# Performance work log

Hardware: AMD Instinct MI355X
Metric: run time of the kernel (lower is better)

## Reference

```python
import jax, jax.numpy as jnp
import numpy as np

D = 768      # d_model
H = 12       # num_heads
L = 2        # num_blocks
N = 3        # number of sequence domains
B = 64       # batch
S = 512      # per-domain sequence length
MULT = 4     # ffn hidden_mult
A = 1        # action_num


def setup_inputs() -> dict:
    key = jax.random.key(0)
    ks = jax.random.split(key, 16)
    def w(k, shape):
        return jax.random.normal(k, shape, jnp.float32) * 0.02
    return {
        "context": jax.random.normal(ks[0], (B, D), jnp.float32),
        "sequences": jax.random.normal(ks[1], (N, B, S, D), jnp.float32),
        "seq_lens": jnp.maximum(jax.random.randint(ks[2], (N, B), 0, S + 1), 1).astype(jnp.int32),
        # per-block (stacked over L) ContextBlock params
        "blk_qn_w": jnp.ones((L, D)), "blk_qn_b": jnp.zeros((L, D)),
        "blk_sn_w": jnp.ones((L, D)), "blk_sn_b": jnp.zeros((L, D)),
        "blk_in_w": w(ks[3], (L, 3 * D, D)), "blk_in_b": jnp.zeros((L, 3 * D)),
        "blk_out_w": w(ks[4], (L, D, D)), "blk_out_b": jnp.zeros((L, D)),
        "blk_gate_w": w(ks[5], (L, D, 2 * D)), "blk_gate_b": jnp.zeros((L, D)),
        "blk_ffn_ln_w": jnp.ones((L, D)), "blk_ffn_ln_b": jnp.zeros((L, D)),
        "blk_ffn_w1": w(ks[6], (L, MULT * D, D)), "blk_ffn_b1": jnp.zeros((L, MULT * D)),
        "blk_ffn_w2": w(ks[7], (L, D, MULT * D)), "blk_ffn_b2": jnp.zeros((L, D)),
        # output norm + classifier
        "out_norm_w": jnp.ones((D,)), "out_norm_b": jnp.zeros((D,)),
        "cls_ln_w": jnp.ones((D,)), "cls_ln_b": jnp.zeros((D,)),
        "cls_w1": w(ks[8], (MULT * D, D)), "cls_b1": jnp.zeros((MULT * D,)),
        "cls_w2": w(ks[9], (A, MULT * D)), "cls_b2": jnp.zeros((A,)),
    }


def _ln(x, w, b):
    m = x.mean(-1, keepdims=True)
    v = ((x - m) ** 2).mean(-1, keepdims=True)
    return (x - m) * jax.lax.rsqrt(v + 1e-5) * w + b


def _forward(context, sequences, pad,
             blk_qn_w, blk_qn_b, blk_sn_w, blk_sn_b,
             blk_in_w, blk_in_b, blk_out_w, blk_out_b,
             blk_gate_w, blk_gate_b,
             blk_ffn_ln_w, blk_ffn_ln_b, blk_ffn_w1, blk_ffn_b1, blk_ffn_w2, blk_ffn_b2,
             out_norm_w, out_norm_b, cls_ln_w, cls_ln_b, cls_w1, cls_b1, cls_w2, cls_b2):
    dh = D // H
    scale = 1.0 / np.sqrt(dh)
    for l in range(L):
        # length-1 query over context; all N domains handled in one batched attention
        q = _ln(context, blk_qn_w[l], blk_qn_b[l])                       # [B, D]
        kv = _ln(sequences, blk_sn_w[l], blk_sn_b[l])                    # [N, B, S, D]
        Wq, Wk, Wv = jnp.split(blk_in_w[l], 3, axis=0)
        bq, bk, bv = jnp.split(blk_in_b[l], 3)
        qh = (q @ Wq.T + bq).reshape(B, H, dh)
        kh = (jnp.einsum('nbsd,ed->nbse', kv, Wk) + bk).reshape(N, B, S, H, dh)
        vh = (jnp.einsum('nbsd,ed->nbse', kv, Wv) + bv).reshape(N, B, S, H, dh)
        scores = jnp.einsum('bhe,nbshe->nbhs', qh, kh) * scale           # [N, B, H, S]
        scores = jnp.where(pad[:, :, None, :], jnp.float32(-1e30), scores)
        attn = jax.nn.softmax(scores, axis=-1)
        ctx = jnp.einsum('nbhs,nbshe->nbhe', attn, vh).reshape(N, B, D)
        attended = ctx @ blk_out_w[l].T + blk_out_b[l]                   # [N, B, D]
        seq_ctx = attended.mean(axis=0)                                  # mean over domains
        gate = jax.nn.sigmoid(jnp.concatenate([context, seq_ctx], axis=-1) @ blk_gate_w[l].T + blk_gate_b[l])
        context = context + gate * seq_ctx
        h = _ln(context, blk_ffn_ln_w[l], blk_ffn_ln_b[l])
        h = jax.nn.silu(h @ blk_ffn_w1[l].T + blk_ffn_b1[l]) @ blk_ffn_w2[l].T + blk_ffn_b2[l]
        context = context + h
    emb = _ln(context, out_norm_w, out_norm_b)
    h = _ln(emb, cls_ln_w, cls_ln_b)
    return jax.nn.silu(h @ cls_w1.T + cls_b1) @ cls_w2.T + cls_b2        # [B, A]


def reference(context, sequences, seq_lens,
              blk_qn_w, blk_qn_b, blk_sn_w, blk_sn_b,
              blk_in_w, blk_in_b, blk_out_w, blk_out_b,
              blk_gate_w, blk_gate_b,
              blk_ffn_ln_w, blk_ffn_ln_b, blk_ffn_w1, blk_ffn_b1, blk_ffn_w2, blk_ffn_b2,
              out_norm_w, out_norm_b, cls_ln_w, cls_ln_b, cls_w1, cls_b1, cls_w2, cls_b2):
    pad = jnp.arange(S)[None, None, :] >= seq_lens[:, :, None]           # [N, B, S], True = padded
    return _forward(context, sequences, pad,
                    blk_qn_w, blk_qn_b, blk_sn_w, blk_sn_b,
                    blk_in_w, blk_in_b, blk_out_w, blk_out_b,
                    blk_gate_w, blk_gate_b,
                    blk_ffn_ln_w, blk_ffn_ln_b, blk_ffn_w1, blk_ffn_b1, blk_ffn_w2, blk_ffn_b2,
                    out_norm_w, out_norm_b, cls_ln_w, cls_ln_b, cls_w1, cls_b1, cls_w2, cls_b2)
```

## Files before the change

### kernel.cpp

```cpp
#include <hip/hip_runtime.h>
#include <hip/hip_bf16.h>
#include <cstdint>

#define DMODEL 768
#define NB 64
#define NHEAD 12
#define DHEAD 64
#define SEQLEN 512
#define NDOM 3
#define NBLK 2
#define FFNH 3072
#define NBROWS (NDOM*NB)
#define NCH 16
#define ROWCH 32

__device__ __forceinline__ float wsum64(float v){
  #pragma unroll
  for (int o = 32; o; o >>= 1) v += __shfl_xor(v, o, 64);
  return v;
}
__device__ __forceinline__ float wmax64(float v){
  #pragma unroll
  for (int o = 32; o; o >>= 1) v = fmaxf(v, __shfl_xor(v, o, 64));
  return v;
}
__device__ __forceinline__ float dot4f(float4 a, float4 b){
  return fmaf(a.x, b.x, fmaf(a.y, b.y, fmaf(a.z, b.z, a.w * b.w)));
}

__global__ __launch_bounds__(256) void k_ln(const float* __restrict__ in,
    const float* __restrict__ w, const float* __restrict__ b,
    float* __restrict__ out, int rows){
  int gw = (blockIdx.x * 256 + threadIdx.x) >> 6;
  int lane = threadIdx.x & 63;
  if (gw >= rows) return;
  const float4* x4 = (const float4*)(in + (size_t)gw * DMODEL);
  float4 v0 = x4[lane], v1 = x4[64 + lane], v2 = x4[128 + lane];
  float s = v0.x+v0.y+v0.z+v0.w + v1.x+v1.y+v1.z+v1.w + v2.x+v2.y+v2.z+v2.w;
  float q = dot4f(v0,v0) + dot4f(v1,v1) + dot4f(v2,v2);
  s = wsum64(s); q = wsum64(q);
  float m = s * (1.0f / DMODEL);
  float var = q * (1.0f / DMODEL) - m * m;
  float r = rsqrtf(var + 1e-5f);
  const float4* w4 = (const float4*)w;
  const float4* b4 = (const float4*)b;
  float4* o4 = (float4*)(out + (size_t)gw * DMODEL);
  float4 vv[3] = {v0, v1, v2};
  #pragma unroll
  for (int seg = 0; seg < 3; ++seg){
    float4 ww = w4[seg*64 + lane], bb = b4[seg*64 + lane], x = vv[seg], o;
    o.x = (x.x - m) * r * ww.x + bb.x;
    o.y = (x.y - m) * r * ww.y + bb.y;
    o.z = (x.z - m) * r * ww.z + bb.z;
    o.w = (x.w - m) * r * ww.w + bb.w;
    o4[seg*64 + lane] = o;
  }
}

__global__ __launch_bounds__(256) void k_ln2(const float* __restrict__ in,
    const float* __restrict__ w1, const float* __restrict__ b1,
    const float* __restrict__ w2, const float* __restrict__ b2,
    float* __restrict__ out, int rows){
  int gw = (blockIdx.x * 256 + threadIdx.x) >> 6;
  int lane = threadIdx.x & 63;
  if (gw >= rows) return;
  const float4* x4 = (const float4*)(in + (size_t)gw * DMODEL);
  float4 vv[3] = {x4[lane], x4[64 + lane], x4[128 + lane]};
  float s = 0, q = 0;
  #pragma unroll
  for (int g = 0; g < 3; ++g){
    s += vv[g].x+vv[g].y+vv[g].z+vv[g].w;
    q += dot4f(vv[g], vv[g]);
  }
  s = wsum64(s); q = wsum64(q);
  float m = s * (1.0f/DMODEL);
  float r = rsqrtf(q * (1.0f/DMODEL) - m*m + 1e-5f);
  const float4* w14 = (const float4*)w1; const float4* b14 = (const float4*)b1;
  float4 yy[3];
  float s2 = 0, q2 = 0;
  #pragma unroll
  for (int g = 0; g < 3; ++g){
    float4 ww = w14[g*64 + lane], bb = b14[g*64 + lane], x = vv[g], o;
    o.x = (x.x - m)*r*ww.x + bb.x; o.y = (x.y - m)*r*ww.y + bb.y;
    o.z = (x.z - m)*r*ww.z + bb.z; o.w = (x.w - m)*r*ww.w + bb.w;
    yy[g] = o;
    s2 += o.x+o.y+o.z+o.w; q2 += dot4f(o,o);
  }
  s2 = wsum64(s2); q2 = wsum64(q2);
  float m2 = s2 * (1.0f/DMODEL);
  float r2 = rsqrtf(q2 * (1.0f/DMODEL) - m2*m2 + 1e-5f);
  const float4* w24 = (const float4*)w2; const float4* b24 = (const float4*)b2;
  float4* o4 = (float4*)(out + (size_t)gw * DMODEL);
  #pragma unroll
  for (int g = 0; g < 3; ++g){
    float4 ww = w24[g*64 + lane], bb = b24[g*64 + lane], y = yy[g], o;
    o.x = (y.x - m2)*r2*ww.x + bb.x; o.y = (y.y - m2)*r2*ww.y + bb.y;
    o.z = (y.z - m2)*r2*ww.z + bb.z; o.w = (y.w - m2)*r2*ww.w + bb.w;
    o4[g*64 + lane] = o;
  }
}

template<int K, int NC, int ACT, bool RES>
__global__ __launch_bounds__(256) void k_gemmW(const float* __restrict__ A,
    const float* __restrict__ W, const float* __restrict__ bias,
    const float* __restrict__ res, float* __restrict__ out){
  int gw = (blockIdx.x * 256 + threadIdx.x) >> 6;
  int lane = threadIdx.x & 63;
  int sl = lane & 7, g = lane >> 3;
  int bg = gw & 7; int j0 = (gw >> 3) * 4;
  const float4* a4 = (const float4*)(A + (size_t)(bg*8 + g) * K);
  const float4* w0 = (const float4*)(W + (size_t)(j0+0) * K);
  const float4* w1 = (const float4*)(W + (size_t)(j0+1) * K);
  const float4* w2 = (const float4*)(W + (size_t)(j0+2) * K);
  const float4* w3 = (const float4*)(W + (size_t)(j0+3) * K);
  float acc0 = 0, acc1 = 0, acc2 = 0, acc3 = 0;
  #pragma unroll 4
  for (int i = 0; i < K/32; ++i){
    float4 av = a4[i*8 + sl];
    acc0 += dot4f(av, w0[i*8 + sl]);
    acc1 += dot4f(av, w1[i*8 + sl]);
    acc2 += dot4f(av, w2[i*8 + sl]);
    acc3 += dot4f(av, w3[i*8 + sl]);
  }
  #pragma unroll
  for (int o = 1; o <= 4; o <<= 1){
    acc0 += __shfl_xor(acc0, o, 64);
    acc1 += __shfl_xor(acc1, o, 64);
    acc2 += __shfl_xor(acc2, o, 64);
    acc3 += __shfl_xor(acc3, o, 64);
  }
  if (sl == 0){
    int row = bg*8 + g;
    float4 bj = *(const float4*)(bias + j0);
    float a[4] = {acc0, acc1, acc2, acc3};
    float bb[4] = {bj.x, bj.y, bj.z, bj.w};
    float v[4];
    #pragma unroll
    for (int u = 0; u < 4; ++u){
      float t = (ACT == 2) ? a[u] * (1.0f/3.0f) + bb[u] : a[u] + bb[u];
      if (ACT == 1) t = t / (1.0f + __expf(-t));
      v[u] = t;
    }
    size_t o = (size_t)row * NC + j0;
    if (RES){
      float4 rr = *(const float4*)(res + o);
      v[0] += rr.x; v[1] += rr.y; v[2] += rr.z; v[3] += rr.w;
    }
    *(float4*)(out + o) = make_float4(v[0], v[1], v[2], v[3]);
  }
}

__global__ __launch_bounds__(256) void k_qpr(const float* __restrict__ qh,
    const float* __restrict__ Wk, const float* __restrict__ snw,
    const float* __restrict__ snb, const float* __restrict__ bk,
    float* __restrict__ QW, float* __restrict__ SQW, float* __restrict__ SC){
  int w = (blockIdx.x * 256 + threadIdx.x) >> 6;
  int lane = threadIdx.x & 63;
  int b = w / NHEAD, h = w - b * NHEAD;
  const float* qrow = qh + (size_t)b * DMODEL + h * DHEAD;
  const float* wbase = Wk + (size_t)h * DHEAD * DMODEL;
  float qp[12] = {};
  for (int e = 0; e < DHEAD; ++e){
    float qv = qrow[e];
    const float* wr = wbase + (size_t)e * DMODEL;
    #pragma unroll
    for (int k = 0; k < 12; ++k) qp[k] = fmaf(qv, wr[k*64 + lane], qp[k]);
  }
  float s1 = 0, s2 = 0;
  float* qwout = QW + (size_t)w * DMODEL;
  #pragma unroll
  for (int k = 0; k < 12; ++k){
    int d = k*64 + lane;
    float q = qp[k];
    float qwv = q * snw[d] * 0.125f;
    qwout[d] = qwv;
    s1 += qwv;
    s2 = fmaf(q, snb[d], s2);
  }
  float s3 = qrow[lane] * bk[h*DHEAD + lane];
  s1 = wsum64(s1); s2 = wsum64(s2); s3 = wsum64(s3);
  if (lane == 0){ SQW[w] = s1; SC[w] = 0.125f * (s2 + s3); }
}

__global__ __launch_bounds__(256, 2) void k_attn4(const float* __restrict__ seq,
    const int* __restrict__ lens, const float* __restrict__ QW,
    const float* __restrict__ SQW, const float* __restrict__ SC,
    float* __restrict__ Pacc, float* __restrict__ Pden,
    float* __restrict__ Pc, float* __restrict__ Pmx){
  int blk = blockIdx.x;
  int ch = blk & (NCH-1); int nb = blk >> 4;
  int wid = threadIdx.x >> 6; int lane = threadIdx.x & 63;
  int b = nb % NB;
  int len = lens[nb];
  int s0 = ch * ROWCH;
  if (s0 >= len) return;
  int send = s0 + ROWCH < len ? s0 + ROWCH : len;
  int h0 = wid * 3;
  size_t pb = (size_t)blk * NHEAD + h0;
  const float4* qwb = (const float4*)(QW + ((size_t)b * NHEAD + h0) * DMODEL);
  float4 q0[3], q1[3], q2[3];
  #pragma unroll
  for (int j = 0; j < 3; ++j){
    q0[j] = qwb[j*(DMODEL/4) + lane];
    q1[j] = qwb[j*(DMODEL/4) + 64 + lane];
    q2[j] = qwb[j*(DMODEL/4) + 128 + lane];
  }
  float sqv[3], scv[3];
  #pragma unroll
  for (int j = 0; j < 3; ++j){ sqv[j] = SQW[b*NHEAD + h0 + j]; scv[j] = SC[b*NHEAD + h0 + j]; }
  float4 a0[3], a1[3], a2[3];
  #pragma unroll
  for (int j = 0; j < 3; ++j){
    a0[j] = make_float4(0,0,0,0); a1[j] = make_float4(0,0,0,0); a2[j] = make_float4(0,0,0,0);
  }
  float den[3] = {0,0,0}, cac[3] = {0,0,0}, mx[3] = {-3.0e38f,-3.0e38f,-3.0e38f};
  const float4* xr = (const float4*)(seq + ((size_t)nb * SEQLEN + s0) * DMODEL);
  float4 x0 = xr[lane], x1 = xr[64 + lane], x2 = xr[128 + lane];
  for (int s = s0; s < send; ++s){
    float4 c0 = x0, c1 = x1, c2 = x2;
    if (s + 1 < send){
      const float4* nx = (const float4*)(seq + ((size_t)nb * SEQLEN + s + 1) * DMODEL);
      x0 = nx[lane]; x1 = nx[64 + lane]; x2 = nx[128 + lane];
    }
    float sm = c0.x+c0.y+c0.z+c0.w + c1.x+c1.y+c1.z+c1.w + c2.x+c2.y+c2.z+c2.w;
    float qq = dot4f(c0,c0) + dot4f(c1,c1) + dot4f(c2,c2);
    float d0 = dot4f(q0[0],c0) + dot4f(q1[0],c1) + dot4f(q2[0],c2);
    float d1 = dot4f(q0[1],c0) + dot4f(q1[1],c1) + dot4f(q2[1],c2);
    float d2 = dot4f(q0[2],c0) + dot4f(q1[2],c1) + dot4f(q2[2],c2);
    sm = wsum64(sm); qq = wsum64(qq);
    d0 = wsum64(d0); d1 = wsum64(d1); d2 = wsum64(d2);
    float m = sm * (1.0f/DMODEL);
    float var = qq * (1.0f/DMODEL) - m * m;
    float r = rsqrtf(var + 1e-5f);
    float dt[3] = {d0, d1, d2};
    #pragma unroll
    for (int j = 0; j < 3; ++j){
      float score = r * (dt[j] - m * sqv[j]) + scv[j];
      if (score > mx[j] + 8.0f){
        float f = __expf(mx[j] - score);
        den[j] *= f; cac[j] *= f;
        a0[j].x*=f; a0[j].y*=f; a0[j].z*=f; a0[j].w*=f;
        a1[j].x*=f; a1[j].y*=f; a1[j].z*=f; a1[j].w*=f;
        a2[j].x*=f; a2[j].y*=f; a2[j].z*=f; a2[j].w*=f;
        mx[j] = score;
      }
      float e = __expf(score - mx[j]);
      float er = e * r;
      a0[j].x = fmaf(er, c0.x, a0[j].x); a0[j].y = fmaf(er, c0.y, a0[j].y);
      a0[j].z = fmaf(er, c0.z, a0[j].z); a0[j].w = fmaf(er, c0.w, a0[j].w);
      a1[j].x = fmaf(er, c1.x, a1[j].x); a1[j].y = fmaf(er, c1.y, a1[j].y);
      a1[j].z = fmaf(er, c1.z, a1[j].z); a1[j].w = fmaf(er, c1.w, a1[j].w);
      a2[j].x = fmaf(er, c2.x, a2[j].x); a2[j].y = fmaf(er, c2.y, a2[j].y);
      a2[j].z = fmaf(er, c2.z, a2[j].z); a2[j].w = fmaf(er, c2.w, a2[j].w);
      den[j] += e;
      cac[j] = fmaf(er, m, cac[j]);
    }
  }
  #pragma unroll
  for (int j = 0; j < 3; ++j){
    float4* pa = (float4*)(Pacc + (pb + j) * DMODEL);
    pa[lane] = a0[j]; pa[64 + lane] = a1[j]; pa[128 + lane] = a2[j];
    if (lane == 0){ Pden[pb+j] = den[j]; Pc[pb+j] = cac[j]; Pmx[pb+j] = mx[j]; }
  }
}

__global__ __launch_bounds__(256) void k_comb(const float* __restrict__ Pacc,
    const float* __restrict__ Pden, const float* __restrict__ Pc,
    const float* __restrict__ Pmx, const int* __restrict__ lens,
    const float* __restrict__ snw, const float* __restrict__ snb,
    float* __restrict__ wsum){
  int tid = blockIdx.x * 256 + threadIdx.x;
  int d = tid % DMODEL;
  int t = tid / DMODEL;
  int h = t % NHEAD;
  int b = t / NHEAD;
  float vec = 0.0f, csum = 0.0f;
  #pragma unroll
  for (int n = 0; n < NDOM; ++n){
    int nb = n*NB + b;
    int len = lens[nb];
    int na = (len + ROWCH - 1) >> 5; if (na > NCH) na = NCH;
    size_t p0 = (size_t)nb * NCH * NHEAD + h;
    float M = -3.0e38f;
    for (int c = 0; c < na; ++c) M = fmaxf(M, Pmx[p0 + (size_t)c*NHEAD]);
    float D = 0, V = 0, C = 0;
    for (int c = 0; c < na; ++c){
      size_t pi = p0 + (size_t)c*NHEAD;
      float w = __expf(Pmx[pi] - M);
      D = fmaf(w, Pden[pi], D);
      V = fmaf(w, Pacc[pi*DMODEL + d], V);
      C = fmaf(w, Pc[pi], C);
    }
    float inv = 1.0f / D;
    vec = fmaf(V, inv, vec);
    csum = fmaf(C, inv, csum);
  }
  wsum[tid] = (vec - csum) * snw[d] + 3.0f * snb[d];
}

__global__ __launch_bounds__(256) void k_ctxv2(const float* __restrict__ wsum,
    const float* __restrict__ Wv, const float* __restrict__ bv, float* __restrict__ ctxsum){
  int gw = (blockIdx.x * 256 + threadIdx.x) >> 6;
  int lane = threadIdx.x & 63;
  int sl = lane & 7, g = lane >> 3;
  int bg = gw & 7; int j0 = (gw >> 3) * 4;
  int h = j0 >> 6;
  const float4* a4 = (const float4*)(wsum + ((size_t)(bg*8 + g) * NHEAD + h) * DMODEL);
  const float4* w0 = (const float4*)(Wv + (size_t)(j0+0) * DMODEL);
  const float4* w1 = (const float4*)(Wv + (size_t)(j0+1) * DMODEL);
  const float4* w2 = (const float4*)(Wv + (size_t)(j0+2) * DMODEL);
  const float4* w3 = (const float4*)(Wv + (size_t)(j0+3) * DMODEL);
  float acc0 = 0, acc1 = 0, acc2 = 0, acc3 = 0;
  #pragma unroll 4
  for (int i = 0; i < DMODEL/32; ++i){
    float4 av = a4[i*8 + sl];
    acc0 += dot4f(av, w0[i*8 + sl]);
    acc1 += dot4f(av, w1[i*8 + sl]);
    acc2 += dot4f(av, w2[i*8 + sl]);
    acc3 += dot4f(av, w3[i*8 + sl]);
  }
  #pragma unroll
  for (int o = 1; o <= 4; o <<= 1){
    acc0 += __shfl_xor(acc0, o, 64);
    acc1 += __shfl_xor(acc1, o, 64);
    acc2 += __shfl_xor(acc2, o, 64);
    acc3 += __shfl_xor(acc3, o, 64);
  }
  if (sl == 0){
    float4 bb = *(const float4*)(bv + j0);
    float4 v = make_float4(acc0 + 3.0f*bb.x, acc1 + 3.0f*bb.y, acc2 + 3.0f*bb.z, acc3 + 3.0f*bb.w);
    *(float4*)(ctxsum + (size_t)(bg*8 + g) * DMODEL + j0) = v;
  }
}

__global__ __launch_bounds__(256) void k_gate2(const float* __restrict__ ctx,
    const float* __restrict__ sctx, const float* __restrict__ Wg,
    const float* __restrict__ gb, float* __restrict__ out){
  int gw = (blockIdx.x * 256 + threadIdx.x) >> 6;
  int lane = threadIdx.x & 63;
  int sl = lane & 7, g = lane >> 3;
  int bg = gw & 7; int j0 = (gw >> 3) * 4;
  int row = bg*8 + g;
  const float4* c4 = (const float4*)(ctx + (size_t)row * DMODEL);
  const float4* s4 = (const float4*)(sctx + (size_t)row * DMODEL);
  const float4* wr0 = (const float4*)(Wg + (size_t)(j0+0) * 2 * DMODEL);
  const float4* wr1 = (const float4*)(Wg + (size_t)(j0+1) * 2 * DMODEL);
  const float4* wr2 = (const float4*)(Wg + (size_t)(j0+2) * 2 * DMODEL);
  const float4* wr3 = (const float4*)(Wg + (size_t)(j0+3) * 2 * DMODEL);
  float acc0 = 0, acc1 = 0, acc2 = 0, acc3 = 0;
  #pragma unroll 4
  for (int i = 0; i < DMODEL/32; ++i){
    float4 cv = c4[i*8 + sl], sv = s4[i*8 + sl];
    acc0 += dot4f(cv, wr0[i*8 + sl]) + dot4f(sv, wr0[192 + i*8 + sl]);
    acc1 += dot4f(cv, wr1[i*8 + sl]) + dot4f(sv, wr1[192 + i*8 + sl]);
    acc2 += dot4f(cv, wr2[i*8 + sl]) + dot4f(sv, wr2[192 + i*8 + sl]);
    acc3 += dot4f(cv, wr3[i*8 + sl]) + dot4f(sv, wr3[192 + i*8 + sl]);
  }
  #pragma unroll
  for (int o = 1; o <= 4; o <<= 1){
    acc0 += __shfl_xor(acc0, o, 64);
    acc1 += __shfl_xor(acc1, o, 64);
    acc2 += __shfl_xor(acc2, o, 64);
    acc3 += __shfl_xor(acc3, o, 64);
  }
  if (sl == 0){
    size_t o = (size_t)row * DMODEL + j0;
    float4 bb = *(const float4*)(gb + j0);
    float4 cc = *(const float4*)(ctx + o);
    float4 ss = *(const float4*)(sctx + o);
    float4 v;
    v.x = cc.x + ss.x / (1.0f + __expf(-(acc0 + bb.x)));
    v.y = cc.y + ss.y / (1.0f + __expf(-(acc1 + bb.y)));
    v.z = cc.z + ss.z / (1.0f + __expf(-(acc2 + bb.z)));
    v.w = cc.w + ss.w / (1.0f + __expf(-(acc3 + bb.w)));
    *(float4*)(out + o) = v;
  }
}

__global__ __launch_bounds__(256) void k_cls2(const float* __restrict__ h2,
    const float* __restrict__ w2, const float* __restrict__ b2, float* __restrict__ out){
  int b = blockIdx.x; int t = threadIdx.x;
  float acc = 0;
  for (int j = t; j < FFNH; j += 256) acc = fmaf(h2[(size_t)b*FFNH + j], w2[j], acc);
  acc = wsum64(acc);
  __shared__ float sh[4];
  if ((t & 63) == 0) sh[t >> 6] = acc;
  __syncthreads();
  if (t == 0) out[b] = sh[0] + sh[1] + sh[2] + sh[3] + b2[0];
}

extern "C" void kernel_launch(void* const* d_in, const int* in_sizes, int n_in,
                              void* d_out, int out_size, void* d_ws, size_t ws_size,
                              hipStream_t stream){
  const float* in_ctx = (const float*)d_in[0];
  const float* seq    = (const float*)d_in[1];
  const int*   lens   = (const int*)d_in[2];
  const float* qn_w   = (const float*)d_in[3];
  const float* qn_b   = (const float*)d_in[4];
  const float* sn_w   = (const float*)d_in[5];
  const float* sn_b   = (const float*)d_in[6];
  const float* in_w   = (const float*)d_in[7];
  const float* in_b   = (const float*)d_in[8];
  const float* out_w  = (const float*)d_in[9];
  const float* out_b  = (const float*)d_in[10];
  const float* gate_w = (const float*)d_in[11];
  const float* gate_b = (const float*)d_in[12];
  const float* fln_w  = (const float*)d_in[13];
  const float* fln_b  = (const float*)d_in[14];
  const float* fw1    = (const float*)d_in[15];
  const float* fb1    = (const float*)d_in[16];
  const float* fw2    = (const float*)d_in[17];
  const float* fb2    = (const float*)d_in[18];
  const float* on_w   = (const float*)d_in[19];
  const float* on_b   = (const float*)d_in[20];
  const float* cl_w   = (const float*)d_in[21];
  const float* cl_b   = (const float*)d_in[22];
  const float* cw1    = (const float*)d_in[23];
  const float* cb1    = (const float*)d_in[24];
  const float* cw2    = (const float*)d_in[25];
  const float* cb2    = (const float*)d_in[26];

  float* wsf = (float*)d_ws;
  size_t off = 0;
  auto alloc = [&](size_t n){ float* p = wsf + off; off += n; return p; };
  float* c0     = alloc((size_t)NB*DMODEL);
  float* c1     = alloc((size_t)NB*DMODEL);
  float* cmid   = alloc((size_t)NB*DMODEL);
  float* qln    = alloc((size_t)NB*DMODEL);
  float* qh     = alloc((size_t)NB*DMODEL);
  float* QW     = alloc((size_t)NB*NHEAD*DMODEL);
  float* SQWb   = alloc((size_t)NB*NHEAD);
  float* SCb    = alloc((size_t)NB*NHEAD);
  float* Pacc   = alloc((size_t)NBROWS*NCH*NHEAD*DMODEL);
  float* Pden   = alloc((size_t)NBROWS*NCH*NHEAD);
  float* Pc     = alloc((size_t)NBROWS*NCH*NHEAD);
  float* Pmx    = alloc((size_t)NBROWS*NCH*NHEAD);
  float* wsumb  = alloc((size_t)NB*NHEAD*DMODEL);
  float* ctxsum = alloc((size_t)NB*DMODEL);
  float* sctx   = alloc((size_t)NB*DMODEL);
  float* h0     = alloc((size_t)NB*DMODEL);
  float* h1     = alloc((size_t)NB*FFNH);
  (void)ws_size; (void)in_sizes; (void)n_in; (void)out_size;

  hipMemcpyAsync(c0, in_ctx, (size_t)NB*DMODEL*sizeof(float), hipMemcpyDeviceToDevice, stream);
  float* cur = c0; float* nxt = c1;

  for (int l = 0; l < NBLK; ++l){
    const float* Wq = in_w + (size_t)l * 3 * DMODEL * DMODEL;
    const float* Wk = Wq + (size_t)DMODEL * DMODEL;
    const float* Wv = Wq + (size_t)2 * DMODEL * DMODEL;
    const float* bq = in_b + (size_t)l * 3 * DMODEL;
    const float* bk = bq + DMODEL;
    const float* bv = bq + 2 * DMODEL;

    k_ln<<<16, 256, 0, stream>>>(cur, qn_w + l*DMODEL, qn_b + l*DMODEL, qln, NB);
    k_gemmW<DMODEL,DMODEL,0,false><<<384, 256, 0, stream>>>(qln, Wq, bq, nullptr, qh);
    k_qpr<<<192, 256, 0, stream>>>(qh, Wk, sn_w + l*DMODEL, sn_b + l*DMODEL, bk, QW, SQWb, SCb);
    k_attn4<<<NBROWS*NCH, 256, 0, stream>>>(seq, lens, QW, SQWb, SCb, Pacc, Pden, Pc, Pmx);
    k_comb<<<(NB*NHEAD*DMODEL)/256, 256, 0, stream>>>(Pacc, Pden, Pc, Pmx, lens, sn_w + l*DMODEL, sn_b + l*DMODEL, wsumb);
    k_ctxv2<<<384, 256, 0, stream>>>(wsumb, Wv, bv, ctxsum);
    k_gemmW<DMODEL,DMODEL,2,false><<<384, 256, 0, stream>>>(ctxsum, out_w + (size_t)l*DMODEL*DMODEL, out_b + l*DMODEL, nullptr, sctx);
    k_gate2<<<384, 256, 0, stream>>>(cur, sctx, gate_w + (size_t)l*DMODEL*2*DMODEL, gate_b + l*DMODEL, cmid);
    k_ln<<<16, 256, 0, stream>>>(cmid, fln_w + l*DMODEL, fln_b + l*DMODEL, h0, NB);
    k_gemmW<DMODEL,FFNH,1,false><<<1536, 256, 0, stream>>>(h0, fw1 + (size_t)l*FFNH*DMODEL, fb1 + l*FFNH, nullptr, h1);
    k_gemmW<FFNH,DMODEL,0,true><<<384, 256, 0, stream>>>(h1, fw2 + (size_t)l*DMODEL*FFNH, fb2 + l*DMODEL, cmid, nxt);
    float* t = cur; cur = nxt; nxt = t;
  }

  k_ln2<<<16, 256, 0, stream>>>(cur, on_w, on_b, cl_w, cl_b, h0, NB);
  k_gemmW<DMODEL,FFNH,1,false><<<1536, 256, 0, stream>>>(h0, cw1, cb1, nullptr, h1);
  k_cls2<<<64, 256, 0, stream>>>(h1, cw2, cb2, (float*)d_out);
}
```

Baseline: 661.4 us.

## Split fused online-softmax attention into score, softmax and PV kernels

Replaces the single-pass online-softmax attention kernel with three kernels: a per-row score kernel computing LayerNorm stats and 12 head scores per thread, a softmax kernel normalizing over full sequences, and a PV kernel accumulating weighted rows with precomputed probabilities. This removes per-row wave shuffle reductions and the rescaling logic, and simplifies the combine step to plain sums. In exchange it adds an extra pass over the sequence data, a scores buffer, and uncoalesced per-thread row reads in the score kernel; chunk size also doubles.

```diff
diff --git a/kernel.cpp b/kernel.cpp
--- a/kernel.cpp
+++ b/kernel.cpp
@@ -11,8 +11,8 @@
 #define NBLK 2
 #define FFNH 3072
 #define NBROWS (NDOM*NB)
-#define NCH 16
-#define ROWCH 32
+#define NCH 8
+#define ROWCH 64
 
 __device__ __forceinline__ float wsum64(float v){
   #pragma unroll
@@ -182,38 +182,102 @@
   if (lane == 0){ SQW[w] = s1; SC[w] = 0.125f * (s2 + s3); }
 }
 
-__global__ __launch_bounds__(256, 2) void k_attn4(const float* __restrict__ seq,
+__global__ __launch_bounds__(256) void k_score(const float* __restrict__ seq,
     const int* __restrict__ lens, const float* __restrict__ QW,
     const float* __restrict__ SQW, const float* __restrict__ SC,
-    float* __restrict__ Pacc, float* __restrict__ Pden,
-    float* __restrict__ Pc, float* __restrict__ Pmx){
+    float* __restrict__ scores, float* __restrict__ mbuf, float* __restrict__ rbuf){
   int blk = blockIdx.x;
-  int ch = blk & (NCH-1); int nb = blk >> 4;
-  int wid = threadIdx.x >> 6; int lane = threadIdx.x & 63;
+  int half = blk & 1, nb = blk >> 1;
+  int wid = threadIdx.x >> 6, lane = threadIdx.x & 63;
+  int len = lens[nb];
+  int s0 = (half*4 + wid) * 64;
+  if (s0 >= len) return;
   int b = nb % NB;
+  int row = s0 + lane;
+  const float4* xr = (const float4*)(seq + ((size_t)nb * SEQLEN + row) * DMODEL);
+  const float4* qw = (const float4*)(QW + (size_t)b * NHEAD * DMODEL);
+  float dt[12];
+  #pragma unroll
+  for (int h = 0; h < 12; ++h) dt[h] = 0.0f;
+  float sm = 0.0f, qq = 0.0f;
+  #pragma unroll 2
+  for (int c = 0; c < 192; ++c){
+    float4 x = xr[c];
+    sm += x.x + x.y + x.z + x.w;
+    qq += dot4f(x, x);
+    #pragma unroll
+    for (int h = 0; h < 12; ++h) dt[h] += dot4f(qw[h*192 + c], x);
+  }
+  float m = sm * (1.0f/DMODEL);
+  float var = qq * (1.0f/DMODEL) - m * m;
+  float r = rsqrtf(var + 1e-5f);
+  mbuf[(size_t)nb*SEQLEN + row] = m;
+  rbuf[(size_t)nb*SEQLEN + row] = r;
+  const float* sqv = SQW + b*NHEAD;
+  const float* scv = SC + b*NHEAD;
+  #pragma unroll
+  for (int h = 0; h < 12; ++h)
+    scores[((size_t)nb*NHEAD + h)*SEQLEN + row] = r * (dt[h] - m * sqv[h]) + scv[h];
+}
+
+__global__ __launch_bounds__(256) void k_softmax(float* __restrict__ scores,
+    const int* __restrict__ lens, const float* __restrict__ mbuf,
+    const float* __restrict__ rbuf, float* __restrict__ cbuf){
+  int row = (blockIdx.x * 256 + threadIdx.x) >> 6;
+  int lane = threadIdx.x & 63;
+  if (row >= NBROWS * NHEAD) return;
+  int nb = row / NHEAD;
+  int len = lens[nb];
+  float* sp = scores + (size_t)row * SEQLEN;
+  float v[8];
+  float mx = -3.0e38f;
+  #pragma unroll
+  for (int i = 0; i < 8; ++i){
+    int s = i*64 + lane;
+    v[i] = sp[s];
+    if (s < len) mx = fmaxf(mx, v[i]);
+  }
+  mx = wmax64(mx);
+  float sum = 0;
+  #pragma unroll
+  for (int i = 0; i < 8; ++i){
+    int s = i*64 + lane;
+    float e = (s < len) ? __expf(v[i] - mx) : 0.0f;
+    v[i] = e; sum += e;
+  }
+  sum = wsum64(sum);
+  float inv = 1.0f / sum;
+  float c = 0;
+  #pragma unroll
+  for (int i = 0; i < 8; ++i){
+    int s = i*64 + lane;
+    float r = (s < len) ? rbuf[(size_t)nb*SEQLEN + s] : 0.0f;
+    float m = (s < len) ? mbuf[(size_t)nb*SEQLEN + s] : 0.0f;
+    float a = v[i] * inv * r;
+    sp[s] = a;
+    c = fmaf(a, m, c);
+  }
+  c = wsum64(c);
+  if (lane == 0) cbuf[row] = c;
+}
+
+__global__ __launch_bounds__(256) void k_pv(const float* __restrict__ seq,
+    const int* __restrict__ lens, const float* __restrict__ er,
+    float* __restrict__ Pacc){
+  int blk = blockIdx.x;
+  int ch = blk & (NCH-1); int nb = blk >> 3;
   int len = lens[nb];
   int s0 = ch * ROWCH;
   if (s0 >= len) return;
   int send = s0 + ROWCH < len ? s0 + ROWCH : len;
+  int wid = threadIdx.x >> 6, lane = threadIdx.x & 63;
   int h0 = wid * 3;
-  size_t pb = (size_t)blk * NHEAD + h0;
-  const float4* qwb = (const float4*)(QW + ((size_t)b * NHEAD + h0) * DMODEL);
-  float4 q0[3], q1[3], q2[3];
-  #pragma unroll
-  for (int j = 0; j < 3; ++j){
-    q0[j] = qwb[j*(DMODEL/4) + lane];
-    q1[j] = qwb[j*(DMODEL/4) + 64 + lane];
-    q2[j] = qwb[j*(DMODEL/4) + 128 + lane];
-  }
-  float sqv[3], scv[3];
-  #pragma unroll
-  for (int j = 0; j < 3; ++j){ sqv[j] = SQW[b*NHEAD + h0 + j]; scv[j] = SC[b*NHEAD + h0 + j]; }
+  const float* e0p = er + ((size_t)nb * NHEAD + h0) * SEQLEN;
   float4 a0[3], a1[3], a2[3];
   #pragma unroll
   for (int j = 0; j < 3; ++j){
     a0[j] = make_float4(0,0,0,0); a1[j] = make_float4(0,0,0,0); a2[j] = make_float4(0,0,0,0);
   }
-  float den[3] = {0,0,0}, cac[3] = {0,0,0}, mx[3] = {-3.0e38f,-3.0e38f,-3.0e38f};
   const float4* xr = (const float4*)(seq + ((size_t)nb * SEQLEN + s0) * DMODEL);
   float4 x0 = xr[lane], x1 = xr[64 + lane], x2 = xr[128 + lane];
   for (int s = s0; s < send; ++s){
@@ -222,51 +286,36 @@
       const float4* nx = (const float4*)(seq + ((size_t)nb * SEQLEN + s + 1) * DMODEL);
       x0 = nx[lane]; x1 = nx[64 + lane]; x2 = nx[128 + lane];
     }
-    float sm = c0.x+c0.y+c0.z+c0.w + c1.x+c1.y+c1.z+c1.w + c2.x+c2.y+c2.z+c2.w;
-    float qq = dot4f(c0,c0) + dot4f(c1,c1) + dot4f(c2,c2);
-    float d0 = dot4f(q0[0],c0) + dot4f(q1[0],c1) + dot4f(q2[0],c2);
-    float d1 = dot4f(q0[1],c0) + dot4f(q1[1],c1) + dot4f(q2[1],c2);
-    float d2 = dot4f(q0[2],c0) + dot4f(q1[2],c1) + dot4f(q2[2],c2);
-    sm = wsum64(sm); qq = wsum64(qq);
-    d0 = wsum64(d0); d1 = wsum64(d1); d2 = wsum64(d2);
-    float m = sm * (1.0f/DMODEL);
-    float var = qq * (1.0f/DMODEL) - m * m;
-    float r = rsqrtf(var + 1e-5f);
-    float dt[3] = {d0, d1, d2};
-    #pragma unroll
-    for (int j = 0; j < 3; ++j){
-      float score = r * (dt[j] - m * sqv[j]) + scv[j];
-      if (score > mx[j] + 8.0f){
-        float f = __expf(mx[j] - score);
-        den[j] *= f; cac[j] *= f;
-        a0[j].x*=f; a0[j].y*=f; a0[j].z*=f; a0[j].w*=f;
-        a1[j].x*=f; a1[j].y*=f; a1[j].z*=f; a1[j].w*=f;
-        a2[j].x*=f; a2[j].y*=f; a2[j].z*=f; a2[j].w*=f;
-        mx[j] = score;
-      }
-      float e = __expf(score - mx[j]);
-      float er = e * r;
-      a0[j].x = fmaf(er, c0.x, a0[j].x); a0[j].y = fmaf(er, c0.y, a0[j].y);
-      a0[j].z = fmaf(er, c0.z, a0[j].z); a0[j].w = fmaf(er, c0.w, a0[j].w);
-      a1[j].x = fmaf(er, c1.x, a1[j].x); a1[j].y = fmaf(er, c1.y, a1[j].y);
-      a1[j].z = fmaf(er, c1.z, a1[j].z); a1[j].w = fmaf(er, c1.w, a1[j].w);
-      a2[j].x = fmaf(er, c2.x, a2[j].x); a2[j].y = fmaf(er, c2.y, a2[j].y);
-      a2[j].z = fmaf(er, c2.z, a2[j].z); a2[j].w = fmaf(er, c2.w, a2[j].w);
-      den[j] += e;
-      cac[j] = fmaf(er, m, cac[j]);
-    }
-  }
+    float e0 = e0p[s], e1 = e0p[SEQLEN + s], e2 = e0p[2*SEQLEN + s];
+    a0[0].x = fmaf(e0, c0.x, a0[0].x); a0[0].y = fmaf(e0, c0.y, a0[0].y);
+    a0[0].z = fmaf(e0, c0.z, a0[0].z); a0[0].w = fmaf(e0, c0.w, a0[0].w);
+    a1[0].x = fmaf(e0, c1.x, a1[0].x); a1[0].y = fmaf(e0, c1.y, a1[0].y);
+    a1[0].z = fmaf(e0, c1.z, a1[0].z); a1[0].w = fmaf(e0, c1.w, a1[0].w);
+    a2[0].x = fmaf(e0, c2.x, a2[0].x); a2[0].y = fmaf(e0, c2.y, a2[0].y);
+    a2[0].z = fmaf(e0, c2.z, a2[0].z); a2[0].w = fmaf(e0, c2.w, a2[0].w);
+    a0[1].x = fmaf(e1, c0.x, a0[1].x); a0[1].y = fmaf(e1, c0.y, a0[1].y);
+    a0[1].z = fmaf(e1, c0.z, a0[1].z); a0[1].w = fmaf(e1, c0.w, a0[1].w);
+    a1[1].x = fmaf(e1, c1.x, a1[1].x); a1[1].y = fmaf(e1, c1.y, a1[1].y);
+    a1[1].z = fmaf(e1, c1.z, a1[1].z); a1[1].w = fmaf(e1, c1.w, a1[1].w);
+    a2[1].x = fmaf(e1, c2.x, a2[1].x); a2[1].y = fmaf(e1, c2.y, a2[1].y);
+    a2[1].z = fmaf(e1, c2.z, a2[1].z); a2[1].w = fmaf(e1, c2.w, a2[1].w);
+    a0[2].x = fmaf(e2, c0.x, a0[2].x); a0[2].y = fmaf(e2, c0.y, a0[2].y);
+    a0[2].z = fmaf(e2, c0.z, a0[2].z); a0[2].w = fmaf(e2, c0.w, a0[2].w);
+    a1[2].x = fmaf(e2, c1.x, a1[2].x); a1[2].y = fmaf(e2, c1.y, a1[2].y);
+    a1[2].z = fmaf(e2, c1.z, a1[2].z); a1[2].w = fmaf(e2, c1.w, a1[2].w);
+    a2[2].x = fmaf(e2, c2.x, a2[2].x); a2[2].y = fmaf(e2, c2.y, a2[2].y);
+    a2[2].z = fmaf(e2, c2.z, a2[2].z); a2[2].w = fmaf(e2, c2.w, a2[2].w);
+  }
+  float* pa = Pacc + ((size_t)blk * NHEAD + h0) * DMODEL;
   #pragma unroll
   for (int j = 0; j < 3; ++j){
-    float4* pa = (float4*)(Pacc + (pb + j) * DMODEL);
-    pa[lane] = a0[j]; pa[64 + lane] = a1[j]; pa[128 + lane] = a2[j];
-    if (lane == 0){ Pden[pb+j] = den[j]; Pc[pb+j] = cac[j]; Pmx[pb+j] = mx[j]; }
+    float4* p = (float4*)(pa + (size_t)j * DMODEL);
+    p[lane] = a0[j]; p[64 + lane] = a1[j]; p[128 + lane] = a2[j];
   }
 }
 
 __global__ __launch_bounds__(256) void k_comb(const float* __restrict__ Pacc,
-    const float* __restrict__ Pden, const float* __restrict__ Pc,
-    const float* __restrict__ Pmx, const int* __restrict__ lens,
+    const float* __restrict__ cbuf, const int* __restrict__ lens,
     const float* __restrict__ snw, const float* __restrict__ snb,
     float* __restrict__ wsum){
   int tid = blockIdx.x * 256 + threadIdx.x;
@@ -279,21 +328,11 @@
   for (int n = 0; n < NDOM; ++n){
     int nb = n*NB + b;
     int len = lens[nb];
-    int na = (len + ROWCH - 1) >> 5; if (na > NCH) na = NCH;
-    size_t p0 = (size_t)nb * NCH * NHEAD + h;
-    float M = -3.0e38f;
-    for (int c = 0; c < na; ++c) M = fmaxf(M, Pmx[p0 + (size_t)c*NHEAD]);
-    float D = 0, V = 0, C = 0;
-    for (int c = 0; c < na; ++c){
-      size_t pi = p0 + (size_t)c*NHEAD;
-      float w = __expf(Pmx[pi] - M);
-      D = fmaf(w, Pden[pi], D);
-      V = fmaf(w, Pacc[pi*DMODEL + d], V);
-      C = fmaf(w, Pc[pi], C);
-    }
-    float inv = 1.0f / D;
-    vec = fmaf(V, inv, vec);
-    csum = fmaf(C, inv, csum);
+    int na = (len + ROWCH - 1) >> 6; if (na > NCH) na = NCH;
+    size_t p0 = ((size_t)nb * NCH * NHEAD + h) * DMODEL + d;
+    for (int c = 0; c < na; ++c)
+      vec += Pacc[p0 + (size_t)c * NHEAD * DMODEL];
+    csum += cbuf[nb*NHEAD + h];
   }
   wsum[tid] = (vec - csum) * snw[d] + 3.0f * snb[d];
 }
@@ -431,10 +470,11 @@
   float* QW     = alloc((size_t)NB*NHEAD*DMODEL);
   float* SQWb   = alloc((size_t)NB*NHEAD);
   float* SCb    = alloc((size_t)NB*NHEAD);
+  float* scores = alloc((size_t)NBROWS*NHEAD*SEQLEN);
+  float* mbuf   = alloc((size_t)NBROWS*SEQLEN);
+  float* rbuf   = alloc((size_t)NBROWS*SEQLEN);
+  float* cbuf   = alloc((size_t)NBROWS*NHEAD);
   float* Pacc   = alloc((size_t)NBROWS*NCH*NHEAD*DMODEL);
-  float* Pden   = alloc((size_t)NBROWS*NCH*NHEAD);
-  float* Pc     = alloc((size_t)NBROWS*NCH*NHEAD);
-  float* Pmx    = alloc((size_t)NBROWS*NCH*NHEAD);
   float* wsumb  = alloc((size_t)NB*NHEAD*DMODEL);
   float* ctxsum = alloc((size_t)NB*DMODEL);
   float* sctx   = alloc((size_t)NB*DMODEL);
@@ -456,8 +496,10 @@
     k_ln<<<16, 256, 0, stream>>>(cur, qn_w + l*DMODEL, qn_b + l*DMODEL, qln, NB);
     k_gemmW<DMODEL,DMODEL,0,false><<<384, 256, 0, stream>>>(qln, Wq, bq, nullptr, qh);
     k_qpr<<<192, 256, 0, stream>>>(qh, Wk, sn_w + l*DMODEL, sn_b + l*DMODEL, bk, QW, SQWb, SCb);
-    k_attn4<<<NBROWS*NCH, 256, 0, stream>>>(seq, lens, QW, SQWb, SCb, Pacc, Pden, Pc, Pmx);
-    k_comb<<<(NB*NHEAD*DMODEL)/256, 256, 0, stream>>>(Pacc, Pden, Pc, Pmx, lens, sn_w + l*DMODEL, sn_b + l*DMODEL, wsumb);
+    k_score<<<NBROWS*2, 256, 0, stream>>>(seq, lens, QW, SQWb, SCb, scores, mbuf, rbuf);
+    k_softmax<<<(NBROWS*NHEAD)/4, 256, 0, stream>>>(scores, lens, mbuf, rbuf, cbuf);
+    k_pv<<<NBROWS*NCH, 256, 0, stream>>>(seq, lens, scores, Pacc);
+    k_comb<<<(NB*NHEAD*DMODEL)/256, 256, 0, stream>>>(Pacc, cbuf, lens, sn_w + l*DMODEL, sn_b + l*DMODEL, wsumb);
     k_ctxv2<<<384, 256, 0, stream>>>(wsumb, Wv, bv, ctxsum);
     k_gemmW<DMODEL,DMODEL,2,false><<<384, 256, 0, stream>>>(ctxsum, out_w + (size_t)l*DMODEL*DMODEL, out_b + l*DMODEL, nullptr, sctx);
     k_gate2<<<384, 256, 0, stream>>>(cur, sctx, gate_w + (size_t)l*DMODEL*2*DMODEL, gate_b + l*DMODEL, cmid);
```

Result: no change. 667.9 us (+1.0%).

## Precompute bf16 sequences and row stats; use MFMA for attention scores

Applied to the files above, without the earlier changes.

Adds a one-time prep kernel that converts the sequence tensor to bf16 and stores per-row LayerNorm mean and rstd, so both blocks reuse them. Attention scores are now computed with bf16 MFMA (16x16x32) over 64-row chunks with heads padded to 16. Softmax is done per chunk with an LDS reduction, followed by a weighted accumulation over bf16 rows. The main intent is to halve the sequence bytes read per block and move the dot products onto matrix cores. The cost is lower precision in the scores and the weighted sums, plus the extra prep pass.

```diff
diff --git a/kernel.cpp b/kernel.cpp
--- a/kernel.cpp
+++ b/kernel.cpp
@@ -11,8 +11,11 @@
 #define NBLK 2
 #define FFNH 3072
 #define NBROWS (NDOM*NB)
-#define NCH 16
-#define ROWCH 32
+#define NCH 8
+#define ROWCH 64
+
+typedef __attribute__((ext_vector_type(8))) short short8;
+typedef __attribute__((ext_vector_type(4))) float f32x4;
 
 __device__ __forceinline__ float wsum64(float v){
   #pragma unroll
@@ -26,6 +29,12 @@
 }
 __device__ __forceinline__ float dot4f(float4 a, float4 b){
   return fmaf(a.x, b.x, fmaf(a.y, b.y, fmaf(a.z, b.z, a.w * b.w)));
+}
+__device__ __forceinline__ uint32_t bfpair(float lo, float hi){
+  uint32_t ul = __float_as_uint(lo), uh = __float_as_uint(hi);
+  ul = (ul + 0x7FFFu + ((ul >> 16) & 1u)) >> 16;
+  uh = (uh + 0x7FFFu + ((uh >> 16) & 1u)) & 0xFFFF0000u;
+  return ul | uh;
 }
 
 __global__ __launch_bounds__(256) void k_ln(const float* __restrict__ in,
@@ -150,117 +159,183 @@
   }
 }
 
+__global__ __launch_bounds__(256) void k_prep(const float* __restrict__ seq,
+    uint32_t* __restrict__ xbf, float* __restrict__ mstat, float* __restrict__ rstat){
+  int gw = (blockIdx.x * 256 + threadIdx.x) >> 6;
+  int lane = threadIdx.x & 63;
+  const float4* x4 = (const float4*)(seq + (size_t)gw * DMODEL);
+  float4 v0 = x4[lane], v1 = x4[64 + lane], v2 = x4[128 + lane];
+  float s = v0.x+v0.y+v0.z+v0.w + v1.x+v1.y+v1.z+v1.w + v2.x+v2.y+v2.z+v2.w;
+  float q = dot4f(v0,v0) + dot4f(v1,v1) + dot4f(v2,v2);
+  s = wsum64(s); q = wsum64(q);
+  float m = s * (1.0f/DMODEL);
+  float r = rsqrtf(q * (1.0f/DMODEL) - m*m + 1e-5f);
+  if (lane == 0){ mstat[gw] = m; rstat[gw] = r; }
+  uint32_t* o = xbf + (size_t)gw * 384;
+  o[2*lane]       = bfpair(v0.x, v0.y);
+  o[2*lane+1]     = bfpair(v0.z, v0.w);
+  o[128+2*lane]   = bfpair(v1.x, v1.y);
+  o[128+2*lane+1] = bfpair(v1.z, v1.w);
+  o[256+2*lane]   = bfpair(v2.x, v2.y);
+  o[256+2*lane+1] = bfpair(v2.z, v2.w);
+}
+
 __global__ __launch_bounds__(256) void k_qpr(const float* __restrict__ qh,
     const float* __restrict__ Wk, const float* __restrict__ snw,
     const float* __restrict__ snb, const float* __restrict__ bk,
-    float* __restrict__ QW, float* __restrict__ SQW, float* __restrict__ SC){
+    uint32_t* __restrict__ QWbf, float* __restrict__ SQW, float* __restrict__ SC){
   int w = (blockIdx.x * 256 + threadIdx.x) >> 6;
   int lane = threadIdx.x & 63;
-  int b = w / NHEAD, h = w - b * NHEAD;
+  int b = w >> 4, h = w & 15;
+  uint32_t* qwout = QWbf + (size_t)w * 384;
+  if (h >= 12){
+    #pragma unroll
+    for (int k = 0; k < 6; ++k) qwout[k*64 + lane] = 0;
+    if (lane == 0){ SQW[w] = 0.0f; SC[w] = 0.0f; }
+    return;
+  }
   const float* qrow = qh + (size_t)b * DMODEL + h * DHEAD;
   const float* wbase = Wk + (size_t)h * DHEAD * DMODEL;
-  float qp[12] = {};
+  float qa[6] = {0,0,0,0,0,0}, qb[6] = {0,0,0,0,0,0};
   for (int e = 0; e < DHEAD; ++e){
     float qv = qrow[e];
-    const float* wr = wbase + (size_t)e * DMODEL;
-    #pragma unroll
-    for (int k = 0; k < 12; ++k) qp[k] = fmaf(qv, wr[k*64 + lane], qp[k]);
+    const float* wr = wbase + (size_t)e * DMODEL + 2*lane;
+    #pragma unroll
+    for (int k = 0; k < 6; ++k){
+      qa[k] = fmaf(qv, wr[k*128], qa[k]);
+      qb[k] = fmaf(qv, wr[k*128 + 1], qb[k]);
+    }
   }
   float s1 = 0, s2 = 0;
-  float* qwout = QW + (size_t)w * DMODEL;
-  #pragma unroll
-  for (int k = 0; k < 12; ++k){
-    int d = k*64 + lane;
-    float q = qp[k];
-    float qwv = q * snw[d] * 0.125f;
-    qwout[d] = qwv;
-    s1 += qwv;
-    s2 = fmaf(q, snb[d], s2);
+  #pragma unroll
+  for (int k = 0; k < 6; ++k){
+    int d0 = k*128 + 2*lane;
+    float va = qa[k] * snw[d0]   * 0.125f;
+    float vb = qb[k] * snw[d0+1] * 0.125f;
+    uint32_t pr = bfpair(va, vb);
+    qwout[k*64 + lane] = pr;
+    s1 += __uint_as_float(pr << 16) + __uint_as_float(pr & 0xFFFF0000u);
+    s2 = fmaf(qa[k], snb[d0], fmaf(qb[k], snb[d0+1], s2));
   }
   float s3 = qrow[lane] * bk[h*DHEAD + lane];
   s1 = wsum64(s1); s2 = wsum64(s2); s3 = wsum64(s3);
   if (lane == 0){ SQW[w] = s1; SC[w] = 0.125f * (s2 + s3); }
 }
 
-__global__ __launch_bounds__(256, 2) void k_attn4(const float* __restrict__ seq,
-    const int* __restrict__ lens, const float* __restrict__ QW,
+__global__ __launch_bounds__(256) void k_attnM(const uint32_t* __restrict__ xbf,
+    const int* __restrict__ lens, const uint32_t* __restrict__ QWbf,
     const float* __restrict__ SQW, const float* __restrict__ SC,
+    const float* __restrict__ mstat, const float* __restrict__ rstat,
     float* __restrict__ Pacc, float* __restrict__ Pden,
     float* __restrict__ Pc, float* __restrict__ Pmx){
+  __shared__ float er_lds[64*17];
+  __shared__ float tmax[4][16], tsum[4][16], tcs[4][16], fls[4][16];
   int blk = blockIdx.x;
-  int ch = blk & (NCH-1); int nb = blk >> 4;
-  int wid = threadIdx.x >> 6; int lane = threadIdx.x & 63;
-  int b = nb % NB;
+  int ch = blk & 7, nb = blk >> 3;
   int len = lens[nb];
   int s0 = ch * ROWCH;
   if (s0 >= len) return;
-  int send = s0 + ROWCH < len ? s0 + ROWCH : len;
+  int b = nb % NB;
+  int tid = threadIdx.x, wid = tid >> 6, lane = tid & 63;
+  int l15 = lane & 15, mg = lane >> 4;
+  int r0 = s0 + wid * 16;
+
+  const short8* ax = (const short8*)(xbf + ((size_t)(nb*SEQLEN + r0 + l15)) * 384) + mg;
+  const short8* bq = (const short8*)(QWbf + ((size_t)(b*16 + l15)) * 384) + mg;
+  f32x4 acc = {0.0f, 0.0f, 0.0f, 0.0f};
+  #pragma unroll
+  for (int kk = 0; kk < 24; ++kk){
+    short8 av = ax[kk*4];
+    short8 bv = bq[kk*4];
+    acc = __builtin_amdgcn_mfma_f32_16x16x32_bf16(av, bv, acc, 0, 0, 0);
+  }
+  float sqw = SQW[b*16 + l15], scc = SC[b*16 + l15];
+  float sco[4];
+  #pragma unroll
+  for (int j = 0; j < 4; ++j){
+    int s = r0 + mg*4 + j;
+    float mm = mstat[(size_t)nb*SEQLEN + s];
+    float v = rstat[(size_t)nb*SEQLEN + s] * (acc[j] - mm * sqw) + scc;
+    sco[j] = (s < len) ? v : -3.0e38f;
+  }
+  float tm = fmaxf(fmaxf(sco[0], sco[1]), fmaxf(sco[2], sco[3]));
+  tm = fmaxf(tm, __shfl_xor(tm, 16, 64));
+  tm = fmaxf(tm, __shfl_xor(tm, 32, 64));
+  float es = 0, cs = 0;
+  #pragma unroll
+  for (int j = 0; j < 4; ++j){
+    int s = r0 + mg*4 + j;
+    float e = (sco[j] > -1.0e37f) ? __expf(sco[j] - tm) : 0.0f;
+    float rr = rstat[(size_t)nb*SEQLEN + s];
+    float er = e * rr;
+    er_lds[(wid*16 + mg*4 + j)*17 + l15] = er;
+    es += e;
+    cs = fmaf(er, mstat[(size_t)nb*SEQLEN + s], cs);
+  }
+  es += __shfl_xor(es, 16, 64); es += __shfl_xor(es, 32, 64);
+  cs += __shfl_xor(cs, 16, 64); cs += __shfl_xor(cs, 32, 64);
+  if (lane < 16){ tmax[wid][lane] = tm; tsum[wid][lane] = es; tcs[wid][lane] = cs; }
+  __syncthreads();
+  if (tid < 16){
+    int hh = tid;
+    float M = fmaxf(fmaxf(tmax[0][hh], tmax[1][hh]), fmaxf(tmax[2][hh], tmax[3][hh]));
+    float D = 0, C = 0;
+    #pragma unroll
+    for (int w = 0; w < 4; ++w){
+      float f = (tmax[w][hh] > -1.0e37f) ? __expf(tmax[w][hh] - M) : 0.0f;
+      fls[w][hh] = f;
+      D = fmaf(f, tsum[w][hh], D);
+      C = fmaf(f, tcs[w][hh], C);
+    }
+    if (hh < NHEAD){
+      Pmx[(size_t)blk*NHEAD + hh] = M;
+      Pden[(size_t)blk*NHEAD + hh] = D;
+      Pc[(size_t)blk*NHEAD + hh] = C;
+    }
+  }
+  __syncthreads();
+  #pragma unroll
+  for (int t = 0; t < 4; ++t){
+    int i = tid + t*256;
+    int row = i >> 4, hh = i & 15;
+    er_lds[row*17 + hh] *= fls[row >> 4][hh];
+  }
+  __syncthreads();
+
   int h0 = wid * 3;
-  size_t pb = (size_t)blk * NHEAD + h0;
-  const float4* qwb = (const float4*)(QW + ((size_t)b * NHEAD + h0) * DMODEL);
-  float4 q0[3], q1[3], q2[3];
+  float a[3][12];
+  #pragma unroll
+  for (int j = 0; j < 3; ++j)
+    #pragma unroll
+    for (int c = 0; c < 12; ++c) a[j][c] = 0.0f;
+  const uint32_t* xr0 = xbf + ((size_t)(nb*SEQLEN + s0)) * 384 + lane*6;
+  int nrows = len - s0; if (nrows > ROWCH) nrows = ROWCH;
+  for (int s = 0; s < nrows; ++s){
+    const uint32_t* xr = xr0 + (size_t)s * 384;
+    uint2 u01 = *(const uint2*)(xr);
+    uint2 u23 = *(const uint2*)(xr + 2);
+    uint2 u45 = *(const uint2*)(xr + 4);
+    float e0 = er_lds[s*17 + h0], e1 = er_lds[s*17 + h0 + 1], e2 = er_lds[s*17 + h0 + 2];
+    float x[12];
+    x[0]  = __uint_as_float(u01.x << 16); x[1]  = __uint_as_float(u01.x & 0xFFFF0000u);
+    x[2]  = __uint_as_float(u01.y << 16); x[3]  = __uint_as_float(u01.y & 0xFFFF0000u);
+    x[4]  = __uint_as_float(u23.x << 16); x[5]  = __uint_as_float(u23.x & 0xFFFF0000u);
+    x[6]  = __uint_as_float(u23.y << 16); x[7]  = __uint_as_float(u23.y & 0xFFFF0000u);
+    x[8]  = __uint_as_float(u45.x << 16); x[9]  = __uint_as_float(u45.x & 0xFFFF0000u);
+    x[10] = __uint_as_float(u45.y << 16); x[11] = __uint_as_float(u45.y & 0xFFFF0000u);
+    #pragma unroll
+    for (int c = 0; c < 12; ++c){
+      a[0][c] = fmaf(e0, x[c], a[0][c]);
+      a[1][c] = fmaf(e1, x[c], a[1][c]);
+      a[2][c] = fmaf(e2, x[c], a[2][c]);
+    }
+  }
   #pragma unroll
   for (int j = 0; j < 3; ++j){
-    q0[j] = qwb[j*(DMODEL/4) + lane];
-    q1[j] = qwb[j*(DMODEL/4) + 64 + lane];
-    q2[j] = qwb[j*(DMODEL/4) + 128 + lane];
-  }
-  float sqv[3], scv[3];
-  #pragma unroll
-  for (int j = 0; j < 3; ++j){ sqv[j] = SQW[b*NHEAD + h0 + j]; scv[j] = SC[b*NHEAD + h0 + j]; }
-  float4 a0[3], a1[3], a2[3];
-  #pragma unroll
-  for (int j = 0; j < 3; ++j){
-    a0[j] = make_float4(0,0,0,0); a1[j] = make_float4(0,0,0,0); a2[j] = make_float4(0,0,0,0);
-  }
-  float den[3] = {0,0,0}, cac[3] = {0,0,0}, mx[3] = {-3.0e38f,-3.0e38f,-3.0e38f};
-  const float4* xr = (const float4*)(seq + ((size_t)nb * SEQLEN + s0) * DMODEL);
-  float4 x0 = xr[lane], x1 = xr[64 + lane], x2 = xr[128 + lane];
-  for (int s = s0; s < send; ++s){
-    float4 c0 = x0, c1 = x1, c2 = x2;
-    if (s + 1 < send){
-      const float4* nx = (const float4*)(seq + ((size_t)nb * SEQLEN + s + 1) * DMODEL);
-      x0 = nx[lane]; x1 = nx[64 + lane]; x2 = nx[128 + lane];
-    }
-    float sm = c0.x+c0.y+c0.z+c0.w + c1.x+c1.y+c1.z+c1.w + c2.x+c2.y+c2.z+c2.w;
-    float qq = dot4f(c0,c0) + dot4f(c1,c1) + dot4f(c2,c2);
-    float d0 = dot4f(q0[0],c0) + dot4f(q1[0],c1) + dot4f(q2[0],c2);
-    float d1 = dot4f(q0[1],c0) + dot4f(q1[1],c1) + dot4f(q2[1],c2);
-    float d2 = dot4f(q0[2],c0) + dot4f(q1[2],c1) + dot4f(q2[2],c2);
-    sm = wsum64(sm); qq = wsum64(qq);
-    d0 = wsum64(d0); d1 = wsum64(d1); d2 = wsum64(d2);
-    float m = sm * (1.0f/DMODEL);
-    float var = qq * (1.0f/DMODEL) - m * m;
-    float r = rsqrtf(var + 1e-5f);
-    float dt[3] = {d0, d1, d2};
-    #pragma unroll
-    for (int j = 0; j < 3; ++j){
-      float score = r * (dt[j] - m * sqv[j]) + scv[j];
-      if (score > mx[j] + 8.0f){
-        float f = __expf(mx[j] - score);
-        den[j] *= f; cac[j] *= f;
-        a0[j].x*=f; a0[j].y*=f; a0[j].z*=f; a0[j].w*=f;
-        a1[j].x*=f; a1[j].y*=f; a1[j].z*=f; a1[j].w*=f;
-        a2[j].x*=f; a2[j].y*=f; a2[j].z*=f; a2[j].w*=f;
-        mx[j] = score;
-      }
-      float e = __expf(score - mx[j]);
-      float er = e * r;
-      a0[j].x = fmaf(er, c0.x, a0[j].x); a0[j].y = fmaf(er, c0.y, a0[j].y);
-      a0[j].z = fmaf(er, c0.z, a0[j].z); a0[j].w = fmaf(er, c0.w, a0[j].w);
-      a1[j].x = fmaf(er, c1.x, a1[j].x); a1[j].y = fmaf(er, c1.y, a1[j].y);
-      a1[j].z = fmaf(er, c1.z, a1[j].z); a1[j].w = fmaf(er, c1.w, a1[j].w);
-      a2[j].x = fmaf(er, c2.x, a2[j].x); a2[j].y = fmaf(er, c2.y, a2[j].y);
-      a2[j].z = fmaf(er, c2.z, a2[j].z); a2[j].w = fmaf(er, c2.w, a2[j].w);
-      den[j] += e;
-      cac[j] = fmaf(er, m, cac[j]);
-    }
-  }
-  #pragma unroll
-  for (int j = 0; j < 3; ++j){
-    float4* pa = (float4*)(Pacc + (pb + j) * DMODEL);
-    pa[lane] = a0[j]; pa[64 + lane] = a1[j]; pa[128 + lane] = a2[j];
-    if (lane == 0){ Pden[pb+j] = den[j]; Pc[pb+j] = cac[j]; Pmx[pb+j] = mx[j]; }
+    float* p = Pacc + ((size_t)blk*NHEAD + h0 + j) * DMODEL + lane*12;
+    #pragma unroll
+    for (int c = 0; c < 12; c += 4)
+      *(float4*)(p + c) = make_float4(a[j][c], a[j][c+1], a[j][c+2], a[j][c+3]);
   }
 }
 
@@ -279,8 +354,8 @@
   for (int n = 0; n < NDOM; ++n){
     int nb = n*NB + b;
     int len = lens[nb];
-    int na = (len + ROWCH - 1) >> 5; if (na > NCH) na = NCH;
-    size_t p0 = (size_t)nb * NCH * NHEAD + h;
+    int na = (len + ROWCH - 1) >> 6; if (na > NCH) na = NCH;
+    size_t p0 = (size_t)(nb * NCH) * NHEAD + h;
     float M = -3.0e38f;
     for (int c = 0; c < na; ++c) M = fmaxf(M, Pmx[p0 + (size_t)c*NHEAD]);
     float D = 0, V = 0, C = 0;
@@ -428,9 +503,12 @@
   float* cmid   = alloc((size_t)NB*DMODEL);
   float* qln    = alloc((size_t)NB*DMODEL);
   float* qh     = alloc((size_t)NB*DMODEL);
-  float* QW     = alloc((size_t)NB*NHEAD*DMODEL);
-  float* SQWb   = alloc((size_t)NB*NHEAD);
-  float* SCb    = alloc((size_t)NB*NHEAD);
+  uint32_t* QWbf = (uint32_t*)alloc((size_t)NB*16*384);
+  float* SQWb   = alloc((size_t)NB*16);
+  float* SCb    = alloc((size_t)NB*16);
+  uint32_t* xbf = (uint32_t*)alloc((size_t)NBROWS*SEQLEN*384);
+  float* mstat  = alloc((size_t)NBROWS*SEQLEN);
+  float* rstat  = alloc((size_t)NBROWS*SEQLEN);
   float* Pacc   = alloc((size_t)NBROWS*NCH*NHEAD*DMODEL);
   float* Pden   = alloc((size_t)NBROWS*NCH*NHEAD);
   float* Pc     = alloc((size_t)NBROWS*NCH*NHEAD);
@@ -443,8 +521,9 @@
   (void)ws_size; (void)in_sizes; (void)n_in; (void)out_size;
 
   hipMemcpyAsync(c0, in_ctx, (size_t)NB*DMODEL*sizeof(float), hipMemcpyDeviceToDevice, stream);
+  k_prep<<<(NBROWS*SEQLEN)/4, 256, 0, stream>>>(seq, xbf, mstat, rstat);
+
   float* cur = c0; float* nxt = c1;
-
   for (int l = 0; l < NBLK; ++l){
     const float* Wq = in_w + (size_t)l * 3 * DMODEL * DMODEL;
     const float* Wk = Wq + (size_t)DMODEL * DMODEL;
@@ -455,8 +534,8 @@
 
     k_ln<<<16, 256, 0, stream>>>(cur, qn_w + l*DMODEL, qn_b + l*DMODEL, qln, NB);
     k_gemmW<DMODEL,DMODEL,0,false><<<384, 256, 0, stream>>>(qln, Wq, bq, nullptr, qh);
-    k_qpr<<<192, 256, 0, stream>>>(qh, Wk, sn_w + l*DMODEL, sn_b + l*DMODEL, bk, QW, SQWb, SCb);
-    k_attn4<<<NBROWS*NCH, 256, 0, stream>>>(seq, lens, QW, SQWb, SCb, Pacc, Pden, Pc, Pmx);
+    k_qpr<<<256, 256, 0, stream>>>(qh, Wk, sn_w + l*DMODEL, sn_b + l*DMODEL, bk, QWbf, SQWb, SCb);
+    k_attnM<<<NBROWS*NCH, 256, 0, stream>>>(xbf, lens, QWbf, SQWb, SCb, mstat, rstat, Pacc, Pden, Pc, Pmx);
     k_comb<<<(NB*NHEAD*DMODEL)/256, 256, 0, stream>>>(Pacc, Pden, Pc, Pmx, lens, sn_w + l*DMODEL, sn_b + l*DMODEL, wsumb);
     k_ctxv2<<<384, 256, 0, stream>>>(wsumb, Wv, bv, ctxsum);
     k_gemmW<DMODEL,DMODEL,2,false><<<384, 256, 0, stream>>>(ctxsum, out_w + (size_t)l*DMODEL*DMODEL, out_b + l*DMODEL, nullptr, sctx);
```

New measurement: 579.6 us. -12.4%, faster.
